# Performance work log

Hardware: AMD Instinct MI355X
Metric: run time of the kernel (lower is better)

The kernel has to match this reference:

```python
import jax, jax.numpy as jnp
import numpy as np
from jax.scipy.linalg import expm

LAMBDA_ORTHO = 1.0


def setup_inputs() -> dict:
    key = jax.random.key(0)
    so8_raw = jax.random.normal(key, (524288, 8, 8), dtype=jnp.float32)
    return {"so8_raw": so8_raw}


def reference(so8_raw):
    # A = 0.5 * (P - P^T): skew-symmetric part per 8x8 block
    A = 0.5 * (so8_raw - jnp.swapaxes(so8_raw, -1, -2))
    # R = expm(A), batched over leading dim via vmap
    R = jax.vmap(expm)(A)
    # ||R^T R - I||_F per block, then mean over blocks
    gram = jnp.einsum('nji,njk->nik', R, R)  # R^T R, [N,8,8]
    err = gram - jnp.eye(8, dtype=R.dtype)
    ortho_err = jnp.sqrt(jnp.sum(err * err, axis=(1, 2))).mean()
    return LAMBDA_ORTHO * ortho_err
```

## Files before the change

kernel.cpp:

```cpp
#include <hip/hip_runtime.h>
#include <math.h>

#pragma clang fp contract(off)

#define MM_USE_FMA 1
#define GRAM_USE_FMA 1
#define POLY_FUSED 1
#define LU_SCALE_DIVIDE 1

__device__ __forceinline__ void mm8(const float* __restrict__ A,
                                    const float* __restrict__ B,
                                    float* __restrict__ C) {
  #pragma unroll
  for (int i = 0; i < 8; ++i) {
    #pragma unroll
    for (int j = 0; j < 8; ++j) {
      float s = A[i*8] * B[j];
      #pragma unroll
      for (int k = 1; k < 8; ++k)
        s = __builtin_fmaf(A[i*8+k], B[k*8+j], s);
      C[i*8+j] = s;
    }
  }
}

__device__ __forceinline__ void mm8_sym(const float* __restrict__ A,
                                        float* __restrict__ C) {
  #pragma unroll
  for (int i = 0; i < 8; ++i) {
    #pragma unroll
    for (int j = i; j < 8; ++j) {
      float s = A[i*8] * A[j];
      #pragma unroll
      for (int k = 1; k < 8; ++k)
        s = __builtin_fmaf(A[i*8+k], A[k*8+j], s);
      C[i*8+j] = s;
      C[j*8+i] = s;
    }
  }
}

__global__ __launch_bounds__(256, 1)
void triality_kernel(const float* __restrict__ in, double* __restrict__ acc)
{
  const int t = blockIdx.x * 256 + threadIdx.x;
  const float4* src = (const float4*)(in + (size_t)t * 64);

  float p[64];
  #pragma unroll
  for (int i = 0; i < 16; ++i) {
    float4 q4 = src[i];
    p[4*i+0] = q4.x; p[4*i+1] = q4.y; p[4*i+2] = q4.z; p[4*i+3] = q4.w;
  }

  float a[64];
  #pragma unroll
  for (int i = 0; i < 8; ++i)
    #pragma unroll
    for (int j = 0; j < 8; ++j)
      a[i*8+j] = 0.5f * (p[i*8+j] - p[j*8+i]);

  float l1 = 0.0f;
  #pragma unroll
  for (int j = 0; j < 8; ++j) {
    float cs = 0.0f;
    #pragma unroll
    for (int i = 0; i < 8; ++i) cs = cs + fabsf(a[i*8+j]);
    l1 = fmaxf(l1, cs);
  }

  float fl = floorf(log2f(l1 / 3.925724783138660f));
  int ns = (fl > 0.0f) ? (int)fl : 0;
  if (ns > 0) {
    float sc = exp2f((float)(-ns));
    #pragma unroll
    for (int e = 0; e < 64; ++e) a[e] = a[e] * sc;
  }

  float a2[64], a4[64], a6[64];
  mm8_sym(a, a2);
  mm8_sym(a2, a4);
  mm8(a4, a2, a6);

  #pragma unroll
  for (int i = 0; i < 8; ++i) {
    #pragma unroll
    for (int j = 0; j < 8; ++j) {
      int e = i*8+j;
      float x6 = a6[e], x4 = a4[e], x2 = a2[e];
      float w = __builtin_fmaf(1512.0f, x4, x6);
      w = __builtin_fmaf(277200.0f, x2, w);
      float v = __builtin_fmaf(56.0f, x6, 25200.0f * x4);
      v = __builtin_fmaf(1995840.0f, x2, v);
      if (i == j) { w = w + 8648640.0f; v = v + 17297280.0f; }
      a6[e] = w; a4[e] = v;
    }
  }

  float u[64];
  mm8(a, a6, u);

  #pragma unroll
  for (int e = 0; e < 64; ++e) {
    float uu = u[e], vv = a4[e];
    u[e]  = uu + vv;
    a6[e] = vv - uu;
  }
  float* P = u;
  float* Q = a6;

  int piv[8];
  #pragma unroll
  for (int k = 0; k < 8; ++k) {
    float amax = fabsf(Q[k*8+k]); int jp = k;
    #pragma unroll
    for (int i = k+1; i < 8; ++i) {
      float av = fabsf(Q[i*8+k]);
      if (av > amax) { amax = av; jp = i; }
    }
    piv[k] = jp;
    #pragma unroll
    for (int i = k+1; i < 8; ++i) {
      bool d = (jp == i);
      #pragma unroll
      for (int j = 0; j < 8; ++j) {
        float x = Q[k*8+j], y = Q[i*8+j];
        Q[k*8+j] = d ? y : x;
        Q[i*8+j] = d ? x : y;
      }
    }
    float dk = Q[k*8+k];
    #pragma unroll
    for (int i = k+1; i < 8; ++i) Q[i*8+k] = Q[i*8+k] / dk;
    #pragma unroll
    for (int i = k+1; i < 8; ++i) {
      float lik = Q[i*8+k];
      #pragma unroll
      for (int j = k+1; j < 8; ++j)
        Q[i*8+j] = __builtin_fmaf(-lik, Q[k*8+j], Q[i*8+j]);
    }
  }

  #pragma unroll
  for (int k = 0; k < 8; ++k) {
    int jp = piv[k];
    #pragma unroll
    for (int i = k+1; i < 8; ++i) {
      bool d = (jp == i);
      #pragma unroll
      for (int j = 0; j < 8; ++j) {
        float x = P[k*8+j], y = P[i*8+j];
        P[k*8+j] = d ? y : x;
        P[i*8+j] = d ? x : y;
      }
    }
  }
  #pragma unroll
  for (int k = 0; k < 8; ++k) {
    #pragma unroll
    for (int i = k+1; i < 8; ++i) {
      float lik = Q[i*8+k];
      #pragma unroll
      for (int j = 0; j < 8; ++j)
        P[i*8+j] = __builtin_fmaf(-lik, P[k*8+j], P[i*8+j]);
    }
  }
  #pragma unroll
  for (int k = 7; k >= 0; --k) {
    float dk = Q[k*8+k];
    #pragma unroll
    for (int j = 0; j < 8; ++j) P[k*8+j] = P[k*8+j] / dk;
    #pragma unroll
    for (int i = 0; i < k; ++i) {
      float uik = Q[i*8+k];
      #pragma unroll
      for (int j = 0; j < 8; ++j)
        P[i*8+j] = __builtin_fmaf(-uik, P[k*8+j], P[i*8+j]);
    }
  }

  for (int sq = 0; sq < ns; ++sq) {
    float t2[64];
    mm8(P, P, t2);
    #pragma unroll
    for (int e = 0; e < 64; ++e) P[e] = t2[e];
  }

  float s2 = 0.0f;
  #pragma unroll
  for (int i = 0; i < 8; ++i) {
    #pragma unroll
    for (int kk = i; kk < 8; ++kk) {
      float g = P[0*8+i] * P[0*8+kk];
      #pragma unroll
      for (int j = 1; j < 8; ++j)
        g = __builtin_fmaf(P[j*8+i], P[j*8+kk], g);
      float e = g - (i == kk ? 1.0f : 0.0f);
      float e2 = e * e;
      s2 = s2 + (i == kk ? e2 : 2.0f * e2);
    }
  }
  float frob = sqrtf(s2);

  double dv = (double)frob;
  #pragma unroll
  for (int off = 32; off > 0; off >>= 1)
    dv += __shfl_down(dv, off);

  __shared__ double part[4];
  const int lane = threadIdx.x & 63;
  const int wid  = threadIdx.x >> 6;
  if (lane == 0) part[wid] = dv;
  __syncthreads();
  if (threadIdx.x == 0) {
    double s = (part[0] + part[1]) + (part[2] + part[3]);
    atomicAdd(acc, s);
  }
}

__global__ void finalize_kernel(const double* __restrict__ acc,
                                float* __restrict__ out, int nmat)
{
  out[0] = (float)(acc[0] / (double)nmat);
}

extern "C" void kernel_launch(void* const* d_in, const int* in_sizes, int n_in,
                              void* d_out, int out_size, void* d_ws, size_t ws_size,
                              hipStream_t stream) {
  const float* in = (const float*)d_in[0];
  float* out = (float*)d_out;
  double* acc = (double*)d_ws;
  int nmat = in_sizes[0] / 64;
  hipMemsetAsync(d_ws, 0, sizeof(double), stream);
  triality_kernel<<<nmat / 256, 256, 0, stream>>>(in, acc);
  finalize_kernel<<<1, 1, 0, stream>>>(acc, out, nmat);
}
```

Measured before the change: 254.4 us.

## Store skew-symmetric and symmetric powers in packed triangular form

Keeps A as 28 upper-triangle entries and A^2, A^4 as 36-entry symmetric packed arrays, exploiting skew-symmetry to skip zero diagonal terms in the A^2 and A*W products. This cuts the register footprint and the FMA count in the Padé polynomial stage. Launch bounds are raised to request two blocks per CU for more occupancy. The risk is extra register spills or a different FMA summation order that slightly changes rounding.

New measurement: 254.0 us. About the same (-0.1%).

```diff
diff --git a/kernel.cpp b/kernel.cpp
--- a/kernel.cpp
+++ b/kernel.cpp
@@ -3,10 +3,13 @@
 
 #pragma clang fp contract(off)
 
-#define MM_USE_FMA 1
-#define GRAM_USE_FMA 1
-#define POLY_FUSED 1
-#define LU_SCALE_DIVIDE 1
+
+__device__ __forceinline__ constexpr int aidx(int i, int j) {
+  return i * (15 - i) / 2 + (j - i - 1);
+}
+__device__ __forceinline__ constexpr int sidx(int i, int j) {
+  return 8 * i - (i * (i - 1)) / 2 + (j - i);
+}
 
 __device__ __forceinline__ void mm8(const float* __restrict__ A,
                                     const float* __restrict__ B,
@@ -24,23 +27,7 @@
   }
 }
 
-__device__ __forceinline__ void mm8_sym(const float* __restrict__ A,
-                                        float* __restrict__ C) {
-  #pragma unroll
-  for (int i = 0; i < 8; ++i) {
-    #pragma unroll
-    for (int j = i; j < 8; ++j) {
-      float s = A[i*8] * A[j];
-      #pragma unroll
-      for (int k = 1; k < 8; ++k)
-        s = __builtin_fmaf(A[i*8+k], A[k*8+j], s);
-      C[i*8+j] = s;
-      C[j*8+i] = s;
-    }
-  }
-}
-
-__global__ __launch_bounds__(256, 1)
+__global__ __launch_bounds__(256, 2)
 void triality_kernel(const float* __restrict__ in, double* __restrict__ acc)
 {
   const int t = blockIdx.x * 256 + threadIdx.x;
@@ -53,19 +40,24 @@
     p[4*i+0] = q4.x; p[4*i+1] = q4.y; p[4*i+2] = q4.z; p[4*i+3] = q4.w;
   }
 
-  float a[64];
+  float au[28];
   #pragma unroll
   for (int i = 0; i < 8; ++i)
     #pragma unroll
-    for (int j = 0; j < 8; ++j)
-      a[i*8+j] = 0.5f * (p[i*8+j] - p[j*8+i]);
+    for (int j = i + 1; j < 8; ++j)
+      au[aidx(i, j)] = 0.5f * (p[i*8+j] - p[j*8+i]);
+
+  auto Aat = [&au](int i, int j) -> float {
+    return (i == j) ? 0.0f : ((i < j) ? au[aidx(i, j)] : -au[aidx(j, i)]);
+  };
 
   float l1 = 0.0f;
   #pragma unroll
   for (int j = 0; j < 8; ++j) {
     float cs = 0.0f;
     #pragma unroll
-    for (int i = 0; i < 8; ++i) cs = cs + fabsf(a[i*8+j]);
+    for (int i = 0; i < 8; ++i)
+      if (i != j) cs = cs + fabsf(Aat(i, j));
     l1 = fmaxf(l1, cs);
   }
 
@@ -74,40 +66,99 @@
   if (ns > 0) {
     float sc = exp2f((float)(-ns));
     #pragma unroll
-    for (int e = 0; e < 64; ++e) a[e] = a[e] * sc;
-  }
-
-  float a2[64], a4[64], a6[64];
-  mm8_sym(a, a2);
-  mm8_sym(a2, a4);
-  mm8(a4, a2, a6);
-
+    for (int e = 0; e < 28; ++e) au[e] = au[e] * sc;
+  }
+
+  float s2[36];
+  #pragma unroll
+  for (int i = 0; i < 8; ++i) {
+    #pragma unroll
+    for (int j = i; j < 8; ++j) {
+      float s = 0.0f; bool first = true;
+      #pragma unroll
+      for (int k = 0; k < 8; ++k) {
+        if (k == i || k == j) continue;
+        float x = Aat(i, k), y = Aat(k, j);
+        if (first) { s = x * y; first = false; }
+        else       { s = __builtin_fmaf(x, y, s); }
+      }
+      s2[sidx(i, j)] = s;
+    }
+  }
+  auto A2 = [&s2](int i, int j) -> float {
+    return (i <= j) ? s2[sidx(i, j)] : s2[sidx(j, i)];
+  };
+
+  float s4[36];
+  #pragma unroll
+  for (int i = 0; i < 8; ++i) {
+    #pragma unroll
+    for (int j = i; j < 8; ++j) {
+      float s = A2(i, 0) * A2(0, j);
+      #pragma unroll
+      for (int k = 1; k < 8; ++k)
+        s = __builtin_fmaf(A2(i, k), A2(k, j), s);
+      s4[sidx(i, j)] = s;
+    }
+  }
+  auto A4 = [&s4](int i, int j) -> float {
+    return (i <= j) ? s4[sidx(i, j)] : s4[sidx(j, i)];
+  };
+
+  float w6[64];
+  #pragma unroll
+  for (int i = 0; i < 8; ++i) {
+    #pragma unroll
+    for (int j = 0; j < 8; ++j) {
+      float s = A4(i, 0) * A2(0, j);
+      #pragma unroll
+      for (int k = 1; k < 8; ++k)
+        s = __builtin_fmaf(A4(i, k), A2(k, j), s);
+      w6[i*8+j] = s;
+    }
+  }
+
+  float vv[64];
   #pragma unroll
   for (int i = 0; i < 8; ++i) {
     #pragma unroll
     for (int j = 0; j < 8; ++j) {
       int e = i*8+j;
-      float x6 = a6[e], x4 = a4[e], x2 = a2[e];
+      float x6 = w6[e], x4 = A4(i, j), x2 = A2(i, j);
       float w = __builtin_fmaf(1512.0f, x4, x6);
       w = __builtin_fmaf(277200.0f, x2, w);
       float v = __builtin_fmaf(56.0f, x6, 25200.0f * x4);
       v = __builtin_fmaf(1995840.0f, x2, v);
       if (i == j) { w = w + 8648640.0f; v = v + 17297280.0f; }
-      a6[e] = w; a4[e] = v;
-    }
-  }
-
-  float u[64];
-  mm8(a, a6, u);
+      w6[e] = w; vv[e] = v;
+    }
+  }
+
+  float uu[64];
+  #pragma unroll
+  for (int i = 0; i < 8; ++i) {
+    #pragma unroll
+    for (int j = 0; j < 8; ++j) {
+      float s = 0.0f; bool first = true;
+      #pragma unroll
+      for (int k = 0; k < 8; ++k) {
+        if (k == i) continue;
+        float x = Aat(i, k), y = w6[k*8+j];
+        if (first) { s = x * y; first = false; }
+        else       { s = __builtin_fmaf(x, y, s); }
+      }
+      uu[i*8+j] = s;
+    }
+  }
 
   #pragma unroll
   for (int e = 0; e < 64; ++e) {
-    float uu = u[e], vv = a4[e];
-    u[e]  = uu + vv;
-    a6[e] = vv - uu;
-  }
-  float* P = u;
-  float* Q = a6;
+    float U = uu[e], V = vv[e];
+    uu[e] = U + V;
+    vv[e] = V - U;
+  }
+  float* P = uu;
+  float* Q = vv;
 
   int piv[8];
   #pragma unroll
@@ -186,7 +237,7 @@
     for (int e = 0; e < 64; ++e) P[e] = t2[e];
   }
 
-  float s2 = 0.0f;
+  float s2acc = 0.0f;
   #pragma unroll
   for (int i = 0; i < 8; ++i) {
     #pragma unroll
@@ -197,10 +248,10 @@
         g = __builtin_fmaf(P[j*8+i], P[j*8+kk], g);
       float e = g - (i == kk ? 1.0f : 0.0f);
       float e2 = e * e;
-      s2 = s2 + (i == kk ? e2 : 2.0f * e2);
-    }
-  }
-  float frob = sqrtf(s2);
+      s2acc = s2acc + (i == kk ? e2 : 2.0f * e2);
+    }
+  }
+  float frob = sqrtf(s2acc);
 
   double dv = (double)frob;
   #pragma unroll
```

## Vectorize 8x8 matmuls and LU solve with packed float2 FMA

Applied to the files above, without the earlier changes.

Stores each 8x8 matrix as 32 float2 pairs and rewrites the matrix products, Pade polynomial, LU forward/back substitution, squaring and Gram computation to use two-wide elementwise FMA, so the compiler can emit packed FP32 instructions (v_pk_fma_f32) and roughly halve the ALU instruction count. It drops the symmetric-product shortcut, so the A^2 and A^4 products and the Gram matrix are now computed in full. It also applies the row pivots to P inside the LU loop instead of in a separate pass. The packed layout can raise register pressure and requires extracting single lanes for pivoting and scalar accesses.

Result: faster. 216.0 us (-15.1%).

```diff
diff --git a/kernel.cpp b/kernel.cpp
--- a/kernel.cpp
+++ b/kernel.cpp
@@ -3,39 +3,25 @@
 
 #pragma clang fp contract(off)
 
-#define MM_USE_FMA 1
-#define GRAM_USE_FMA 1
-#define POLY_FUSED 1
-#define LU_SCALE_DIVIDE 1
-
-__device__ __forceinline__ void mm8(const float* __restrict__ A,
-                                    const float* __restrict__ B,
-                                    float* __restrict__ C) {
+typedef float f2 __attribute__((ext_vector_type(2)));
+
+static __device__ __forceinline__ f2 sp(float x) { f2 r; r.x = x; r.y = x; return r; }
+#define FMA2(A, B, C) __builtin_elementwise_fma((A), (B), (C))
+
+#define EL(m, i, j) (m[(i)*4 + ((j) >> 1)][(j) & 1])
+
+__device__ __forceinline__ void mm8p(const f2* __restrict__ A,
+                                     const f2* __restrict__ B,
+                                     f2* __restrict__ C) {
   #pragma unroll
   for (int i = 0; i < 8; ++i) {
     #pragma unroll
-    for (int j = 0; j < 8; ++j) {
-      float s = A[i*8] * B[j];
-      #pragma unroll
-      for (int k = 1; k < 8; ++k)
-        s = __builtin_fmaf(A[i*8+k], B[k*8+j], s);
-      C[i*8+j] = s;
-    }
-  }
-}
-
-__device__ __forceinline__ void mm8_sym(const float* __restrict__ A,
-                                        float* __restrict__ C) {
-  #pragma unroll
-  for (int i = 0; i < 8; ++i) {
-    #pragma unroll
-    for (int j = i; j < 8; ++j) {
-      float s = A[i*8] * A[j];
-      #pragma unroll
-      for (int k = 1; k < 8; ++k)
-        s = __builtin_fmaf(A[i*8+k], A[k*8+j], s);
-      C[i*8+j] = s;
-      C[j*8+i] = s;
+    for (int c = 0; c < 4; ++c) {
+      f2 s = sp(EL(A, i, 0)) * B[0*4 + c];
+      #pragma unroll
+      for (int k = 1; k < 8; ++k)
+        s = FMA2(sp(EL(A, i, k)), B[k*4 + c], s);
+      C[i*4 + c] = s;
     }
   }
 }
@@ -53,154 +39,176 @@
     p[4*i+0] = q4.x; p[4*i+1] = q4.y; p[4*i+2] = q4.z; p[4*i+3] = q4.w;
   }
 
-  float a[64];
+  f2 aa[32];
   #pragma unroll
   for (int i = 0; i < 8; ++i)
     #pragma unroll
     for (int j = 0; j < 8; ++j)
-      a[i*8+j] = 0.5f * (p[i*8+j] - p[j*8+i]);
+      EL(aa, i, j) = 0.5f * (p[i*8+j] - p[j*8+i]);
 
   float l1 = 0.0f;
   #pragma unroll
   for (int j = 0; j < 8; ++j) {
     float cs = 0.0f;
     #pragma unroll
-    for (int i = 0; i < 8; ++i) cs = cs + fabsf(a[i*8+j]);
+    for (int i = 0; i < 8; ++i) cs = cs + fabsf(EL(aa, i, j));
     l1 = fmaxf(l1, cs);
   }
 
   float fl = floorf(log2f(l1 / 3.925724783138660f));
   int ns = (fl > 0.0f) ? (int)fl : 0;
   if (ns > 0) {
-    float sc = exp2f((float)(-ns));
-    #pragma unroll
-    for (int e = 0; e < 64; ++e) a[e] = a[e] * sc;
-  }
-
-  float a2[64], a4[64], a6[64];
-  mm8_sym(a, a2);
-  mm8_sym(a2, a4);
-  mm8(a4, a2, a6);
-
+    f2 sc = sp(exp2f((float)(-ns)));
+    #pragma unroll
+    for (int e = 0; e < 32; ++e) aa[e] = aa[e] * sc;
+  }
+
+  f2 a2[32];
+  #pragma unroll
+  for (int i = 0; i < 8; ++i)
+    #pragma unroll
+    for (int c = 0; c < 4; ++c) {
+      f2 s = sp(EL(aa, i, 0)) * aa[0*4 + c];
+      #pragma unroll
+      for (int k = 1; k < 8; ++k)
+        s = FMA2(sp(EL(aa, i, k)), aa[k*4 + c], s);
+      a2[i*4 + c] = s;
+    }
+
+  f2 a4[32];
+  #pragma unroll
+  for (int i = 0; i < 8; ++i)
+    #pragma unroll
+    for (int c = 0; c < 4; ++c) {
+      f2 s = sp(EL(a2, i, 0)) * a2[0*4 + c];
+      #pragma unroll
+      for (int k = 1; k < 8; ++k)
+        s = FMA2(sp(EL(a2, i, k)), a2[k*4 + c], s);
+      a4[i*4 + c] = s;
+    }
+
+  f2 w6[32];
+  #pragma unroll
+  for (int i = 0; i < 8; ++i)
+    #pragma unroll
+    for (int c = 0; c < 4; ++c) {
+      f2 s = sp(EL(a4, i, 0)) * a2[0*4 + c];
+      #pragma unroll
+      for (int k = 1; k < 8; ++k)
+        s = FMA2(sp(EL(a4, i, k)), a2[k*4 + c], s);
+      w6[i*4 + c] = s;
+    }
+
+  f2 vv[32];
+  #pragma unroll
+  for (int e = 0; e < 32; ++e) {
+    f2 x6 = w6[e], x4 = a4[e], x2 = a2[e];
+    f2 w = FMA2(sp(1512.0f), x4, x6);
+    w = FMA2(sp(277200.0f), x2, w);
+    f2 v = FMA2(sp(56.0f), x6, sp(25200.0f) * x4);
+    v = FMA2(sp(1995840.0f), x2, v);
+    w6[e] = w; vv[e] = v;
+  }
   #pragma unroll
   for (int i = 0; i < 8; ++i) {
-    #pragma unroll
-    for (int j = 0; j < 8; ++j) {
-      int e = i*8+j;
-      float x6 = a6[e], x4 = a4[e], x2 = a2[e];
-      float w = __builtin_fmaf(1512.0f, x4, x6);
-      w = __builtin_fmaf(277200.0f, x2, w);
-      float v = __builtin_fmaf(56.0f, x6, 25200.0f * x4);
-      v = __builtin_fmaf(1995840.0f, x2, v);
-      if (i == j) { w = w + 8648640.0f; v = v + 17297280.0f; }
-      a6[e] = w; a4[e] = v;
-    }
-  }
-
-  float u[64];
-  mm8(a, a6, u);
-
-  #pragma unroll
-  for (int e = 0; e < 64; ++e) {
-    float uu = u[e], vv = a4[e];
-    u[e]  = uu + vv;
-    a6[e] = vv - uu;
-  }
-  float* P = u;
-  float* Q = a6;
-
-  int piv[8];
+    EL(w6, i, i) = EL(w6, i, i) + 8648640.0f;
+    EL(vv, i, i) = EL(vv, i, i) + 17297280.0f;
+  }
+
+  f2 uu[32];
+  #pragma unroll
+  for (int i = 0; i < 8; ++i)
+    #pragma unroll
+    for (int c = 0; c < 4; ++c) {
+      f2 s = sp(EL(aa, i, 0)) * w6[0*4 + c];
+      #pragma unroll
+      for (int k = 1; k < 8; ++k)
+        s = FMA2(sp(EL(aa, i, k)), w6[k*4 + c], s);
+      uu[i*4 + c] = s;
+    }
+
+  #pragma unroll
+  for (int e = 0; e < 32; ++e) {
+    f2 U = uu[e], V = vv[e];
+    uu[e] = U + V;
+    vv[e] = V - U;
+  }
+  f2* P = uu;
+  f2* Q = vv;
+
   #pragma unroll
   for (int k = 0; k < 8; ++k) {
-    float amax = fabsf(Q[k*8+k]); int jp = k;
+    float amax = fabsf(EL(Q, k, k)); int jp = k;
     #pragma unroll
     for (int i = k+1; i < 8; ++i) {
-      float av = fabsf(Q[i*8+k]);
+      float av = fabsf(EL(Q, i, k));
       if (av > amax) { amax = av; jp = i; }
     }
-    piv[k] = jp;
     #pragma unroll
     for (int i = k+1; i < 8; ++i) {
       bool d = (jp == i);
       #pragma unroll
       for (int j = 0; j < 8; ++j) {
-        float x = Q[k*8+j], y = Q[i*8+j];
-        Q[k*8+j] = d ? y : x;
-        Q[i*8+j] = d ? x : y;
+        float x = EL(Q, k, j), y = EL(Q, i, j);
+        EL(Q, k, j) = d ? y : x;
+        EL(Q, i, j) = d ? x : y;
+        float px = EL(P, k, j), py = EL(P, i, j);
+        EL(P, k, j) = d ? py : px;
+        EL(P, i, j) = d ? px : py;
       }
     }
-    float dk = Q[k*8+k];
-    #pragma unroll
-    for (int i = k+1; i < 8; ++i) Q[i*8+k] = Q[i*8+k] / dk;
+    float dk = EL(Q, k, k);
+    #pragma unroll
+    for (int i = k+1; i < 8; ++i) EL(Q, i, k) = EL(Q, i, k) / dk;
     #pragma unroll
     for (int i = k+1; i < 8; ++i) {
-      float lik = Q[i*8+k];
+      float lik = EL(Q, i, k);
       #pragma unroll
       for (int j = k+1; j < 8; ++j)
-        Q[i*8+j] = __builtin_fmaf(-lik, Q[k*8+j], Q[i*8+j]);
-    }
-  }
-
-  #pragma unroll
-  for (int k = 0; k < 8; ++k) {
-    int jp = piv[k];
-    #pragma unroll
-    for (int i = k+1; i < 8; ++i) {
-      bool d = (jp == i);
-      #pragma unroll
-      for (int j = 0; j < 8; ++j) {
-        float x = P[k*8+j], y = P[i*8+j];
-        P[k*8+j] = d ? y : x;
-        P[i*8+j] = d ? x : y;
-      }
-    }
-  }
-  #pragma unroll
-  for (int k = 0; k < 8; ++k) {
-    #pragma unroll
-    for (int i = k+1; i < 8; ++i) {
-      float lik = Q[i*8+k];
-      #pragma unroll
-      for (int j = 0; j < 8; ++j)
-        P[i*8+j] = __builtin_fmaf(-lik, P[k*8+j], P[i*8+j]);
-    }
-  }
+        EL(Q, i, j) = __builtin_fmaf(-lik, EL(Q, k, j), EL(Q, i, j));
+      f2 nl = sp(-lik);
+      #pragma unroll
+      for (int c = 0; c < 4; ++c)
+        P[i*4 + c] = FMA2(nl, P[k*4 + c], P[i*4 + c]);
+    }
+  }
+
   #pragma unroll
   for (int k = 7; k >= 0; --k) {
-    float dk = Q[k*8+k];
-    #pragma unroll
-    for (int j = 0; j < 8; ++j) P[k*8+j] = P[k*8+j] / dk;
+    float dk = EL(Q, k, k);
+    #pragma unroll
+    for (int j = 0; j < 8; ++j) EL(P, k, j) = EL(P, k, j) / dk;
     #pragma unroll
     for (int i = 0; i < k; ++i) {
-      float uik = Q[i*8+k];
-      #pragma unroll
-      for (int j = 0; j < 8; ++j)
-        P[i*8+j] = __builtin_fmaf(-uik, P[k*8+j], P[i*8+j]);
+      f2 nu = sp(-EL(Q, i, k));
+      #pragma unroll
+      for (int c = 0; c < 4; ++c)
+        P[i*4 + c] = FMA2(nu, P[k*4 + c], P[i*4 + c]);
     }
   }
 
   for (int sq = 0; sq < ns; ++sq) {
-    float t2[64];
-    mm8(P, P, t2);
-    #pragma unroll
-    for (int e = 0; e < 64; ++e) P[e] = t2[e];
-  }
-
-  float s2 = 0.0f;
+    f2 t2[32];
+    mm8p(P, P, t2);
+    #pragma unroll
+    for (int e = 0; e < 32; ++e) P[e] = t2[e];
+  }
+
+  f2 s2p = sp(0.0f);
   #pragma unroll
   for (int i = 0; i < 8; ++i) {
     #pragma unroll
-    for (int kk = i; kk < 8; ++kk) {
-      float g = P[0*8+i] * P[0*8+kk];
+    for (int c = 0; c < 4; ++c) {
+      f2 g = sp(EL(P, 0, i)) * P[0*4 + c];
       #pragma unroll
       for (int j = 1; j < 8; ++j)
-        g = __builtin_fmaf(P[j*8+i], P[j*8+kk], g);
-      float e = g - (i == kk ? 1.0f : 0.0f);
-      float e2 = e * e;
-      s2 = s2 + (i == kk ? e2 : 2.0f * e2);
-    }
-  }
-  float frob = sqrtf(s2);
+        g = FMA2(sp(EL(P, j, i)), P[j*4 + c], g);
+      f2 idv; idv.x = (2*c == i) ? 1.0f : 0.0f; idv.y = (2*c + 1 == i) ? 1.0f : 0.0f;
+      f2 e = g - idv;
+      s2p = FMA2(e, e, s2p);
+    }
+  }
+  float frob = sqrtf(s2p.x + s2p.y);
 
   double dv = (double)frob;
   #pragma unroll
```
